# Performance work log

Hardware: AMD Instinct MI355X
Metric: run time of the kernel (lower is better)

Reference implementation:

```python
import jax, jax.numpy as jnp
import numpy as np

B, N, D = 4, 1024, 1024
H, DH = 16, 64            # heads, dim_head; inner_dim = H*DH = D
CTX_N, CTX_D = 77, 768    # CLIP text context
FF_IN, FF_HID = 8 * D, 4 * D  # GEGLU: proj to 2*4*D, gate to 4*D
EPS = 1e-5
SCALE = DH ** -0.5
NL = 256                  # 2**8 levels for all quantizers
ZP_QKV = 128.0            # asymmetric 8-bit zero point for q/k/v
ZP_W = 0.0                # always_zero=True for softmax-weight quantizer


def _round_ste(t):
    return t + jax.lax.stop_gradient(jnp.round(t) - t)


def _fake_quant(x, delta, zp):
    xq = jnp.clip(_round_ste(x / delta) + zp, 0.0, NL - 1.0)
    return (xq - zp) * delta


def _ln(x, w, b):
    m = x.mean(-1, keepdims=True)
    v = x.var(-1, keepdims=True)
    return (x - m) * jax.lax.rsqrt(v + EPS) * w + b


def _split_heads(t):  # [b, n, h*d] -> [b, h, n, d]
    b, n, _ = t.shape
    return t.reshape(b, n, H, DH).transpose(0, 2, 1, 3)


def _attn(x, ctx, wq, wk, wv, wo, bo, dq, dk, dv, dw):
    q = _split_heads(x @ wq)
    k = _split_heads(ctx @ wk)
    v = _split_heads(ctx @ wv)
    qq = _fake_quant(q, dq, ZP_QKV)
    kk = _fake_quant(k, dk, ZP_QKV)
    sim = jnp.einsum('bhid,bhjd->bhij', qq, kk) * SCALE
    attn = jax.nn.softmax(sim, axis=-1)
    aw = _fake_quant(attn, dw, ZP_W)
    vv = _fake_quant(v, dv, ZP_QKV)
    out = jnp.einsum('bhij,bhjd->bhid', aw, vv)
    b, _, n, _ = out.shape
    out = out.transpose(0, 2, 1, 3).reshape(b, n, H * DH)
    return out @ wo + bo


def _geglu_ff(x, w1, b1, w2, b2):
    h = x @ w1 + b1
    a, g = jnp.split(h, 2, axis=-1)
    return (a * jax.nn.gelu(g, approximate=False)) @ w2 + b2


def setup_inputs() -> dict:
    key = jax.random.key(0)
    ks = jax.random.split(key, 16)
    w = lambda i, shp, s: jax.random.normal(ks[i], shp, jnp.float32) * s
    sD = D ** -0.5
    sC = CTX_D ** -0.5
    return {
        'x': jax.random.normal(ks[0], (B, N, D), jnp.float32),
        'context': jax.random.normal(ks[1], (B, CTX_N, CTX_D), jnp.float32),
        'norm1_w': jnp.ones((D,), jnp.float32), 'norm1_b': jnp.zeros((D,), jnp.float32),
        'norm2_w': jnp.ones((D,), jnp.float32), 'norm2_b': jnp.zeros((D,), jnp.float32),
        'norm3_w': jnp.ones((D,), jnp.float32), 'norm3_b': jnp.zeros((D,), jnp.float32),
        'a1_wq': w(2, (D, D), sD), 'a1_wk': w(3, (D, D), sD), 'a1_wv': w(4, (D, D), sD),
        'a1_wo': w(5, (D, D), sD), 'a1_bo': jnp.zeros((D,), jnp.float32),
        'a2_wq': w(6, (D, D), sD), 'a2_wk': w(7, (CTX_D, D), sC), 'a2_wv': w(8, (CTX_D, D), sC),
        'a2_wo': w(9, (D, D), sD), 'a2_bo': jnp.zeros((D,), jnp.float32),
        'ff_w1': w(10, (D, FF_IN), sD), 'ff_b1': jnp.zeros((FF_IN,), jnp.float32),
        'ff_w2': w(11, (FF_HID, D), FF_HID ** -0.5), 'ff_b2': jnp.zeros((D,), jnp.float32),
        'd1_q': jnp.asarray(0.02, jnp.float32), 'd1_k': jnp.asarray(0.02, jnp.float32),
        'd1_v': jnp.asarray(0.02, jnp.float32), 'd1_w': jnp.asarray(1.0 / 255.0, jnp.float32),
        'd2_q': jnp.asarray(0.02, jnp.float32), 'd2_k': jnp.asarray(0.02, jnp.float32),
        'd2_v': jnp.asarray(0.02, jnp.float32), 'd2_w': jnp.asarray(1.0 / 255.0, jnp.float32),
    }


def reference(x, context, norm1_w, norm1_b, norm2_w, norm2_b, norm3_w, norm3_b,
              a1_wq, a1_wk, a1_wv, a1_wo, a1_bo,
              a2_wq, a2_wk, a2_wv, a2_wo, a2_bo,
              ff_w1, ff_b1, ff_w2, ff_b2,
              d1_q, d1_k, d1_v, d1_w, d2_q, d2_k, d2_v, d2_w):
    # attn1: quantized self-attention
    x = _attn(_ln(x, norm1_w, norm1_b), _ln(x, norm1_w, norm1_b),
              a1_wq, a1_wk, a1_wv, a1_wo, a1_bo, d1_q, d1_k, d1_v, d1_w) + x
    # attn2: quantized cross-attention with text context
    x = _attn(_ln(x, norm2_w, norm2_b), context,
              a2_wq, a2_wk, a2_wv, a2_wo, a2_bo, d2_q, d2_k, d2_v, d2_w) + x
    # GEGLU feed-forward
    x = _geglu_ff(_ln(x, norm3_w, norm3_b), ff_w1, ff_b1, ff_w2, ff_b2) + x
    return x
```

## Files before the change

### kernel.cpp

```cpp
#include <hip/hip_runtime.h>
#include <math.h>


typedef unsigned short u16;
typedef __attribute__((ext_vector_type(8))) short short8;
typedef __attribute__((ext_vector_type(4))) float f32x4;

__device__ inline float b2f(u16 v) { return __uint_as_float(((unsigned)v) << 16); }
__device__ inline u16 f2b(float f) {
  unsigned u = __float_as_uint(f);
  unsigned r = u + 0x7fffu + ((u >> 16) & 1u);
  return (u16)(r >> 16);
}

__device__ inline void glds16(const u16* g, u16* l) {
  __builtin_amdgcn_global_load_lds(
      (const __attribute__((address_space(1))) void*)g,
      (__attribute__((address_space(3))) void*)l, 16, 0, 0);
}

__global__ __launch_bounds__(256) void transpose_k(const float* __restrict__ in,
                                                   u16* __restrict__ out,
                                                   int R, int C) {
  __shared__ float t[32][33];
  int tx = threadIdx.x & 31, ty = threadIdx.x >> 5;
  int c0 = blockIdx.x * 32, r0 = blockIdx.y * 32;
#pragma unroll
  for (int i = 0; i < 32; i += 8)
    t[ty + i][tx] = in[(size_t)(r0 + ty + i) * C + c0 + tx];
  __syncthreads();
#pragma unroll
  for (int i = 0; i < 32; i += 8)
    out[(size_t)(c0 + ty + i) * R + r0 + tx] = f2b(t[tx][ty + i]);
}

struct TrBatch { const float* in[4]; u16* out[4]; int R[4]; };
__global__ __launch_bounds__(256) void transpose4_k(TrBatch a) {
  int z = blockIdx.z;
  const float* in = a.in[z];
  u16* out = a.out[z];
  int R = a.R[z];
  int r0 = blockIdx.y * 32;
  if (r0 >= R) return;
  __shared__ float t[32][33];
  int tx = threadIdx.x & 31, ty = threadIdx.x >> 5;
  int c0 = blockIdx.x * 32;
#pragma unroll
  for (int i = 0; i < 32; i += 8)
    t[ty + i][tx] = in[(size_t)(r0 + ty + i) * 1024 + c0 + tx];
  __syncthreads();
#pragma unroll
  for (int i = 0; i < 32; i += 8)
    out[(size_t)(c0 + ty + i) * R + r0 + tx] = f2b(t[tx][ty + i]);
}

__global__ __launch_bounds__(256) void tr16_k(const u16* __restrict__ in,
                                              u16* __restrict__ out, int NK,
                                              int NKP) {
  __shared__ u16 t[32][33];
  int tx = threadIdx.x & 31, ty = threadIdx.x >> 5;
  int n0 = blockIdx.x * 32, c0 = blockIdx.y * 32, b = blockIdx.z;
  const u16* ib = in + (size_t)b * NK * 1024;
  u16* ob = out + (size_t)b * 1024 * NKP;
#pragma unroll
  for (int i = 0; i < 32; i += 8) {
    int n = n0 + ty + i;
    n = n < NK ? n : NK - 1;
    t[ty + i][tx] = ib[(size_t)n * 1024 + c0 + tx];
  }
  __syncthreads();
#pragma unroll
  for (int i = 0; i < 32; i += 8)
    ob[(size_t)(c0 + ty + i) * NKP + n0 + tx] = t[tx][ty + i];
}

__global__ __launch_bounds__(256) void cast_k(const float* __restrict__ in,
                                              u16* __restrict__ out) {
  int i = (blockIdx.x * 256 + threadIdx.x) * 4;
  float4 v = *(const float4*)(in + i);
  out[i + 0] = f2b(v.x);
  out[i + 1] = f2b(v.y);
  out[i + 2] = f2b(v.z);
  out[i + 3] = f2b(v.w);
}

__global__ __launch_bounds__(256) void ln_k(const float* __restrict__ X,
                                            const float* __restrict__ W,
                                            const float* __restrict__ Bi,
                                            u16* __restrict__ Out) {
  const int row = blockIdx.x, tid = threadIdx.x;
  float4 x = *(const float4*)(X + (size_t)row * 1024 + tid * 4);
  float s = x.x + x.y + x.z + x.w;
  float s2 = x.x * x.x + x.y * x.y + x.z * x.z + x.w * x.w;
#pragma unroll
  for (int off = 32; off >= 1; off >>= 1) {
    s += __shfl_down(s, off);
    s2 += __shfl_down(s2, off);
  }
  __shared__ float red[8];
  int wave = tid >> 6, lane = tid & 63;
  if (lane == 0) { red[wave] = s; red[4 + wave] = s2; }
  __syncthreads();
  s = red[0] + red[1] + red[2] + red[3];
  s2 = red[4] + red[5] + red[6] + red[7];
  float mean = s * 0.0009765625f;
  float var = s2 * 0.0009765625f - mean * mean;
  float rs = rsqrtf(var + 1e-5f);
  float4 w = *(const float4*)(W + tid * 4);
  float4 b = *(const float4*)(Bi + tid * 4);
  u16* orow = Out + (size_t)row * 1024 + tid * 4;
  orow[0] = f2b((x.x - mean) * rs * w.x + b.x);
  orow[1] = f2b((x.y - mean) * rs * w.y + b.y);
  orow[2] = f2b((x.z - mean) * rs * w.z + b.z);
  orow[3] = f2b((x.w - mean) * rs * w.w + b.w);
}

template <int EPI, int TM>
__global__ __launch_bounds__(256, 2) void gemm_bt(
    const u16* __restrict__ A, int lda, const u16* __restrict__ Bt, int ldb,
    void* __restrict__ Cp, int ldc, const float* __restrict__ bias,
    const float* __restrict__ res, int ldr, const float* __restrict__ dp,
    const float* __restrict__ dp2, const float* __restrict__ dp3,
    size_t segsz, int M, int N, int K) {
  __shared__ __align__(16) u16 As[TM * 64];
  __shared__ __align__(16) u16 Bs[128 * 64];
  const int tid = threadIdx.x;
  const int lane = tid & 63, wave = tid >> 6;
  const int qd = lane >> 4, cl = lane & 15;
  const int wm = (wave & 1) * (TM / 2), wn = (wave >> 1) << 6;
  const int m0 = blockIdx.x * TM, n0 = blockIdx.y * 128;

  f32x4 acc[TM / 32][4];
  const f32x4 zero = {0.f, 0.f, 0.f, 0.f};
#pragma unroll
  for (int i = 0; i < TM / 32; i++)
#pragma unroll
    for (int j = 0; j < 4; j++) acc[i][j] = zero;

  for (int k0 = 0; k0 < K; k0 += 64) {
    __syncthreads();
#pragma unroll
    for (int it = 0; it < TM / 32; ++it) {
      int ch = it * 256 + tid;
      int r = ch >> 3, cc = (ch & 7) << 3;
      int gr = m0 + r;
      gr = gr < M ? gr : M - 1;
      glds16(A + (size_t)gr * lda + k0 + cc, As + ch * 8);
    }
#pragma unroll
    for (int it = 0; it < 4; ++it) {
      int ch = it * 256 + tid;
      int r = ch >> 3, cc = (ch & 7) << 3;
      glds16(Bt + (size_t)(n0 + r) * ldb + k0 + cc, Bs + ch * 8);
    }
    __syncthreads();
#pragma unroll
    for (int ks = 0; ks < 64; ks += 32) {
      short8 af[TM / 32], bf[4];
#pragma unroll
      for (int t = 0; t < TM / 32; t++)
        af[t] = *(const short8*)(As + (wm + t * 16 + cl) * 64 + ks + qd * 8);
#pragma unroll
      for (int t = 0; t < 4; t++)
        bf[t] = *(const short8*)(Bs + (wn + t * 16 + cl) * 64 + ks + qd * 8);
#pragma unroll
      for (int mt = 0; mt < TM / 32; mt++)
#pragma unroll
        for (int nt = 0; nt < 4; nt++)
          acc[mt][nt] = __builtin_amdgcn_mfma_f32_16x16x32_bf16(
              af[mt], bf[nt], acc[mt][nt], 0, 0, 0);
    }
  }

  float dscale = 1.f;
  u16* qbase = (u16*)Cp;
  if constexpr (EPI == 0) dscale = 1.0f / dp[0];
  if constexpr (EPI == 2) {
    int seg = n0 >> 10;
    const float* ds = (seg == 0) ? dp : ((seg == 1) ? dp2 : dp3);
    dscale = 1.0f / ds[0];
    qbase = (u16*)Cp + (size_t)seg * segsz;
  }
#pragma unroll
  for (int mt = 0; mt < TM / 32; ++mt) {
#pragma unroll
    for (int r = 0; r < 4; ++r) {
      int row = m0 + wm + mt * 16 + qd * 4 + r;
      if (row >= M) continue;
#pragma unroll
      for (int nt = 0; nt < 4; ++nt) {
        int col = n0 + wn + nt * 16 + cl;
        float v = acc[mt][nt][r];
        if constexpr (EPI == 0) {
          float xq = rintf(v * dscale) + 128.f;
          xq = fminf(fmaxf(xq, 0.f), 255.f);
          qbase[(size_t)row * ldc + col] = f2b(xq - 128.f);
        } else if constexpr (EPI == 2) {
          float xq = rintf(v * dscale) + 128.f;
          xq = fminf(fmaxf(xq, 0.f), 255.f);
          qbase[(size_t)row * ldc + (col & 1023)] = f2b(xq - 128.f);
        } else {
          v += bias[col] + res[(size_t)row * ldr + col];
          ((float*)Cp)[(size_t)row * ldc + col] = v;
        }
      }
    }
  }
}

#define VMW(n) asm volatile("s_waitcnt vmcnt(" #n ")" ::: "memory")
#define LGKM0() asm volatile("s_waitcnt lgkmcnt(0)" ::: "memory")
#define SBAR() __builtin_amdgcn_s_barrier()
#define SCHED0() __builtin_amdgcn_sched_barrier(0)

#define ST_A(P, MH, K0)                                                      \
  do {                                                                       \
    _Pragma("unroll") for (int it = 0; it < 2; ++it) {                       \
      int r_ = (MH) * 128 + it * 64 + sr;                                    \
      glds16(Ag + (size_t)(m0 + r_) * 1024 + (K0) + ((sc ^ (r_ & 7)) << 3),  \
             As + (P) * 16384 + r_ * 64 + (sc << 3));                        \
    }                                                                        \
  } while (0)

#define ST_B(P, BH, K0)                                                      \
  do {                                                                       \
    _Pragma("unroll") for (int it = 0; it < 2; ++it) {                       \
      int r_ = it * 64 + sr;                                                 \
      glds16(W1t + (size_t)((BH) * 4096 + n0 + r_) * 1024 + (K0) +           \
                 ((sc ^ (r_ & 7)) << 3),                                     \
             Bs + (P) * 16384 + ((BH) * 128 + r_) * 64 + (sc << 3));         \
    }                                                                        \
  } while (0)

#define RD_A(P, MH)                                                          \
  do {                                                                       \
    _Pragma("unroll") for (int mf = 0; mf < 4; ++mf) {                       \
      int row_ = (MH) * 128 + wr * 64 + mf * 16 + cl;                        \
      _Pragma("unroll") for (int ks = 0; ks < 2; ++ks)                       \
        af[mf * 2 + ks] = *(const short8*)(As + (P) * 16384 + row_ * 64 +    \
                                           (((ks * 4 + qd) ^ (cl & 7)) << 3)); \
    }                                                                        \
  } while (0)

#define RD_B(P, NH)                                                          \
  do {                                                                       \
    _Pragma("unroll") for (int nf = 0; nf < 2; ++nf) {                       \
      int j_ = (NH) * 128 + wc * 32 + nf * 16 + cl;                          \
      _Pragma("unroll") for (int ks = 0; ks < 2; ++ks)                       \
        bf[nf * 2 + ks] = *(const short8*)(Bs + (P) * 16384 + j_ * 64 +      \
                                           (((ks * 4 + qd) ^ (cl & 7)) << 3)); \
    }                                                                        \
  } while (0)

#define MFMA_Q(MH, NH)                                                       \
  do {                                                                       \
    _Pragma("unroll") for (int mf = 0; mf < 4; ++mf)                         \
      _Pragma("unroll") for (int nf = 0; nf < 2; ++nf)                       \
        _Pragma("unroll") for (int ks = 0; ks < 2; ++ks)                     \
          acc[(MH) * 4 + mf][(NH) * 2 + nf] =                                \
              __builtin_amdgcn_mfma_f32_16x16x32_bf16(                       \
                  af[mf * 2 + ks], bf[nf * 2 + ks],                          \
                  acc[(MH) * 4 + mf][(NH) * 2 + nf], 0, 0, 0);               \
  } while (0)

#define KTILE(P, KN, LAST)                                                   \
  do {                                                                       \
                                            \
    RD_A(P, 0);                                                              \
    RD_B(P, 0);                                                              \
    if (!(LAST)) ST_A((P) ^ 1, 0, KN);                                       \
    SBAR();                                                                  \
    LGKM0();                                                                 \
    SCHED0();                                                                \
    __builtin_amdgcn_s_setprio(1);                                           \
    MFMA_Q(0, 0);                                                            \
    __builtin_amdgcn_s_setprio(0);                                           \
    SCHED0();                                                                \
    if (!(LAST)) { VMW(4); } else { VMW(2); }                                \
    SBAR();                                                                  \
                              \
    RD_A(P, 1);                                                              \
    if (!(LAST)) ST_B((P) ^ 1, 0, KN);                                       \
    SBAR();                                                                  \
    LGKM0();                                                                 \
    SCHED0();                                                                \
    __builtin_amdgcn_s_setprio(1);                                           \
    MFMA_Q(1, 0);                                                            \
    __builtin_amdgcn_s_setprio(0);                                           \
    SCHED0();                                                                \
    if (!(LAST)) { VMW(4); } else { VMW(0); }                                \
    SBAR();                                                                  \
                              \
    RD_B(P, 1);                                                              \
    if (!(LAST)) ST_A((P) ^ 1, 1, KN);                                       \
    SBAR();                                                                  \
    LGKM0();                                                                 \
    SCHED0();                                                                \
    __builtin_amdgcn_s_setprio(1);                                           \
    MFMA_Q(1, 1);                                                            \
    __builtin_amdgcn_s_setprio(0);                                           \
    SCHED0();                                                                \
    SBAR();                                                                  \
             \
    RD_A(P, 0);                                                              \
    if (!(LAST)) ST_B((P) ^ 1, 1, KN);                                       \
    SBAR();                                                                  \
    LGKM0();                                                                 \
    SCHED0();                                                                \
    __builtin_amdgcn_s_setprio(1);                                           \
    MFMA_Q(0, 1);                                                            \
    __builtin_amdgcn_s_setprio(0);                                           \
    SCHED0();                                                                \
    if (!(LAST)) { VMW(4); }                                                 \
    SBAR();                                                                  \
  } while (0)

__global__ __launch_bounds__(512, 1) void ff1_geglu8_k(
    const u16* __restrict__ Ag, const u16* __restrict__ W1t,
    const float* __restrict__ b1, u16* __restrict__ gg) {
  __shared__ __align__(16) u16 smem[65536];
  u16* As = smem;
  u16* Bs = smem + 32768;
  const int tid = threadIdx.x;
  const int lane = tid & 63, wave = tid >> 6;
  const int qd = lane >> 4, cl = lane & 15;
  const int wr = wave >> 2, wc = wave & 3;
  const int m0 = blockIdx.x * 256;
  const int n0 = blockIdx.y * 128;
  const int sr = tid >> 3, sc = tid & 7;

  f32x4 acc[8][4];
  const f32x4 zero = {0.f, 0.f, 0.f, 0.f};
#pragma unroll
  for (int i = 0; i < 8; ++i)
#pragma unroll
    for (int j = 0; j < 4; ++j) acc[i][j] = zero;
  short8 af[8], bf[4];

  ST_A(0, 0, 0);
  ST_B(0, 0, 0);
  ST_A(0, 1, 0);
  ST_B(0, 1, 0);
  VMW(4);
  SBAR();
  SCHED0();

  int p = 0;
#pragma unroll 1
  for (int t = 0; t < 15; ++t) {
    KTILE(p, (t + 1) * 64, 0);
    p ^= 1;
  }
  KTILE(1, 0, 1);

#pragma unroll
  for (int i = 0; i < 8; ++i) {
    const int row = m0 + (i >> 2) * 128 + wr * 64 + (i & 3) * 16 + qd * 4;
#pragma unroll
    for (int nf = 0; nf < 2; ++nf) {
      const int col = n0 + wc * 32 + nf * 16 + cl;
      const float ba = b1[col];
      const float bg = b1[4096 + col];
#pragma unroll
      for (int r = 0; r < 4; ++r) {
        float a = acc[i][nf][r] + ba;
        float g = acc[i][2 + nf][r] + bg;
        float ge = 0.5f * g * (1.0f + erff(g * 0.70710678118654752f));
        gg[(size_t)(row + r) * 4096 + col] = f2b(a * ge);
      }
    }
  }
}

__global__ __launch_bounds__(256, 4) void attn_k(
    const u16* __restrict__ Q, const u16* __restrict__ Kb,
    const u16* __restrict__ VbT, u16* __restrict__ O,
    const float* dqp, const float* dkp, const float* dvp, const float* dwp,
    int NK, int NKP) {
  __shared__ __align__(16) u16 Ks[64 * 64];
  __shared__ __align__(16) u16 VTs[64 * 64];
  __shared__ __align__(16) u16 Ps[4][16 * 72];
  const int tid = threadIdx.x;
  const int lane = tid & 63, wave = tid >> 6;
  const int qd = lane >> 4, cl = lane & 15;
  const int b = blockIdx.z, h = blockIdx.y, qt = blockIdx.x;
  const float sscale = dqp[0] * dkp[0] * 0.125f;
  const float oscale = dwp[0] * dvp[0];
  const float inv_dw = 1.0f / dwp[0];
  const f32x4 zero = {0.f, 0.f, 0.f, 0.f};

  short8 qf[2][2];
#pragma unroll
  for (int g = 0; g < 2; ++g) {
    const u16* qrow =
        Q + (size_t)(b * 1024 + qt * 128 + g * 64 + wave * 16 + cl) * 1024 +
        h * 64;
    qf[g][0] = *(const short8*)(qrow + qd * 8);
    qf[g][1] = *(const short8*)(qrow + 32 + qd * 8);
  }

  const u16* kbase = Kb + (size_t)(b * NK) * 1024 + h * 64;
  const u16* vtbase = VbT + ((size_t)b * 1024 + h * 64) * NKP;
  const int r_st = tid >> 3, c_st = (tid & 7) << 3;

  float m_s[2] = {-1e30f, -1e30f}, l_s[2] = {0.f, 0.f};
  for (int j0 = 0; j0 < NK; j0 += 64) {
    __syncthreads();
#pragma unroll
    for (int it = 0; it < 2; ++it) {
      int r = it * 32 + r_st;
      int j = j0 + r;
      j = j < NK ? j : NK - 1;
      glds16(kbase + (size_t)j * 1024 + c_st, Ks + (it * 256 + tid) * 8);
    }
    __syncthreads();
    const bool full = (j0 + 64 <= NK);
#pragma unroll
    for (int g = 0; g < 2; ++g) {
      float sc[16];
#pragma unroll
      for (int nt = 0; nt < 4; ++nt) {
        short8 kf0 = *(const short8*)(Ks + (nt * 16 + cl) * 64 + qd * 8);
        short8 kf1 = *(const short8*)(Ks + (nt * 16 + cl) * 64 + 32 + qd * 8);
        f32x4 st = zero;
        st = __builtin_amdgcn_mfma_f32_16x16x32_bf16(kf0, qf[g][0], st, 0, 0, 0);
        st = __builtin_amdgcn_mfma_f32_16x16x32_bf16(kf1, qf[g][1], st, 0, 0, 0);
#pragma unroll
        for (int r = 0; r < 4; ++r) {
          int key = j0 + nt * 16 + qd * 4 + r;
          sc[nt * 4 + r] = (full || key < NK) ? st[r] * sscale : -1e30f;
        }
      }
      float mx = sc[0];
#pragma unroll
      for (int i = 1; i < 16; ++i) mx = fmaxf(mx, sc[i]);
      mx = fmaxf(mx, __shfl_xor(mx, 16));
      mx = fmaxf(mx, __shfl_xor(mx, 32));
      float mn = fmaxf(m_s[g], mx);
      float ss = 0.f;
#pragma unroll
      for (int i = 0; i < 16; ++i) ss += __expf(sc[i] - mn);
      ss += __shfl_xor(ss, 16);
      ss += __shfl_xor(ss, 32);
      l_s[g] = l_s[g] * __expf(m_s[g] - mn) + ss;
      m_s[g] = mn;
    }
  }
  float il_s[2] = {1.0f / l_s[0], 1.0f / l_s[1]};

  f32x4 oacc[2][4];
#pragma unroll
  for (int g = 0; g < 2; ++g)
#pragma unroll
    for (int t = 0; t < 4; t++) oacc[g][t] = zero;

  for (int j0 = 0; j0 < NK; j0 += 64) {
    __syncthreads();
#pragma unroll
    for (int it = 0; it < 2; ++it) {
      int r = it * 32 + r_st;
      int j = j0 + r;
      j = j < NK ? j : NK - 1;
      glds16(kbase + (size_t)j * 1024 + c_st, Ks + (it * 256 + tid) * 8);
      glds16(vtbase + (size_t)r * NKP + j0 + c_st, VTs + (it * 256 + tid) * 8);
    }
    __syncthreads();
    const bool full = (j0 + 64 <= NK);
#pragma unroll
    for (int g = 0; g < 2; ++g) {
#pragma unroll
      for (int nt = 0; nt < 4; ++nt) {
        short8 kf0 = *(const short8*)(Ks + (nt * 16 + cl) * 64 + qd * 8);
        short8 kf1 = *(const short8*)(Ks + (nt * 16 + cl) * 64 + 32 + qd * 8);
        f32x4 st = zero;
        st = __builtin_amdgcn_mfma_f32_16x16x32_bf16(kf0, qf[g][0], st, 0, 0, 0);
        st = __builtin_amdgcn_mfma_f32_16x16x32_bf16(kf1, qf[g][1], st, 0, 0, 0);
        u16 pk[4];
#pragma unroll
        for (int r = 0; r < 4; ++r) {
          int key = j0 + nt * 16 + qd * 4 + r;
          float aw = 0.f;
          if (full || key < NK) {
            float attn = __expf(st[r] * sscale - m_s[g]) * il_s[g];
            aw = fminf(fmaxf(rintf(attn * inv_dw), 0.f), 255.f);
          }
          pk[r] = f2b(aw);
        }
        uint2 pv;
        pv.x = (unsigned)pk[0] | ((unsigned)pk[1] << 16);
        pv.y = (unsigned)pk[2] | ((unsigned)pk[3] << 16);
        *(uint2*)(&Ps[wave][cl * 72 + nt * 16 + qd * 4]) = pv;
      }
#pragma unroll
      for (int ks = 0; ks < 2; ++ks) {
        short8 pf = *(const short8*)(&Ps[wave][cl * 72 + ks * 32 + qd * 8]);
#pragma unroll
        for (int dt = 0; dt < 4; ++dt) {
          short8 vf =
              *(const short8*)(VTs + (dt * 16 + cl) * 64 + ks * 32 + qd * 8);
          oacc[g][dt] = __builtin_amdgcn_mfma_f32_16x16x32_bf16(
              pf, vf, oacc[g][dt], 0, 0, 0);
        }
      }
    }
  }
#pragma unroll
  for (int g = 0; g < 2; ++g)
#pragma unroll
    for (int dt = 0; dt < 4; ++dt)
#pragma unroll
      for (int r = 0; r < 4; r++) {
        size_t addr = (size_t)(b * 1024 + qt * 128 + g * 64 + wave * 16 +
                               qd * 4 + r) * 1024 +
                      h * 64 + dt * 16 + cl;
        O[addr] = f2b(oacc[g][dt][r] * oscale);
      }
}

extern "C" void kernel_launch(void* const* d_in, const int* in_sizes, int n_in,
                              void* d_out, int out_size, void* d_ws,
                              size_t ws_size, hipStream_t stream) {
  (void)in_sizes; (void)n_in; (void)out_size; (void)ws_size;
  const float* x    = (const float*)d_in[0];
  const float* ctx  = (const float*)d_in[1];
  const float* n1w  = (const float*)d_in[2];
  const float* n1b  = (const float*)d_in[3];
  const float* n2w  = (const float*)d_in[4];
  const float* n2b  = (const float*)d_in[5];
  const float* n3w  = (const float*)d_in[6];
  const float* n3b  = (const float*)d_in[7];
  const float* a1wq = (const float*)d_in[8];
  const float* a1wk = (const float*)d_in[9];
  const float* a1wv = (const float*)d_in[10];
  const float* a1wo = (const float*)d_in[11];
  const float* a1bo = (const float*)d_in[12];
  const float* a2wq = (const float*)d_in[13];
  const float* a2wk = (const float*)d_in[14];
  const float* a2wv = (const float*)d_in[15];
  const float* a2wo = (const float*)d_in[16];
  const float* a2bo = (const float*)d_in[17];
  const float* ffw1 = (const float*)d_in[18];
  const float* ffb1 = (const float*)d_in[19];
  const float* ffw2 = (const float*)d_in[20];
  const float* ffb2 = (const float*)d_in[21];
  const float* d1q = (const float*)d_in[22];
  const float* d1k = (const float*)d_in[23];
  const float* d1v = (const float*)d_in[24];
  const float* d1w = (const float*)d_in[25];
  const float* d2q = (const float*)d_in[26];
  const float* d2k = (const float*)d_in[27];
  const float* d2v = (const float*)d_in[28];
  const float* d2w = (const float*)d_in[29];

  char* ws = (char*)d_ws;
  const size_t MB = 1u << 20;
  u16* W    = (u16*)(ws + 0 * MB);
  u16* lnb  = (u16*)(ws + 16 * MB);
  u16* qb   = (u16*)(ws + 24 * MB);
  u16* kb   = (u16*)(ws + 32 * MB);
  u16* vb   = (u16*)(ws + 40 * MB);
  u16* vbT  = (u16*)(ws + 48 * MB);
  u16* ao   = (u16*)(ws + 56 * MB);
  float* x1 = (float*)(ws + 64 * MB);
  u16* k2b  = (u16*)(ws + 32 * MB);
  u16* v2b  = k2b + 308 * 1024;
  u16* vbTc = (u16*)(ws + 34 * MB);
  u16* ctxb = (u16*)(ws + 35 * MB);
  u16* gg   = (u16*)(ws + 24 * MB);

  u16* WT0 = W;
  u16* WT1 = (u16*)(ws + 2 * MB);
  u16* WT2 = (u16*)(ws + 4 * MB);
  u16* WT3 = (u16*)(ws + 6 * MB);
  u16* WT3c = WT2 + 1024 * 768;

  dim3 T256(256);
  {
    TrBatch tb;
    tb.in[0] = a1wq; tb.out[0] = WT0; tb.R[0] = 1024;
    tb.in[1] = a1wk; tb.out[1] = WT1; tb.R[1] = 1024;
    tb.in[2] = a1wv; tb.out[2] = WT2; tb.R[2] = 1024;
    tb.in[3] = a1wo; tb.out[3] = WT3; tb.R[3] = 1024;
    transpose4_k<<<dim3(32, 32, 4), T256, 0, stream>>>(tb);
  }
  ln_k<<<4096, T256, 0, stream>>>(x, n1w, n1b, lnb);
  gemm_bt<2, 128><<<dim3(32, 24), T256, 0, stream>>>(
      lnb, 1024, WT0, 1024, qb, 1024, nullptr, nullptr, 0, d1q, d1k, d1v,
      (size_t)4096 * 1024, 4096, 3072, 1024);
  tr16_k<<<dim3(32, 32, 4), T256, 0, stream>>>(vb, vbT, 1024, 1024);
  attn_k<<<dim3(8, 16, 4), T256, 0, stream>>>(qb, kb, vbT, ao, d1q, d1k, d1v,
                                              d1w, 1024, 1024);
  gemm_bt<1, 64><<<dim3(64, 8), T256, 0, stream>>>(
      ao, 1024, WT3, 1024, x1, 1024, a1bo, x, 1024, nullptr, nullptr, nullptr,
      0, 4096, 1024, 1024);
  {
    TrBatch tb;
    tb.in[0] = a2wq; tb.out[0] = WT0; tb.R[0] = 1024;
    tb.in[1] = a2wo; tb.out[1] = WT1; tb.R[1] = 1024;
    tb.in[2] = a2wk; tb.out[2] = WT2;  tb.R[2] = 768;
    tb.in[3] = a2wv; tb.out[3] = WT3c; tb.R[3] = 768;
    transpose4_k<<<dim3(32, 32, 4), T256, 0, stream>>>(tb);
  }
  ln_k<<<4096, T256, 0, stream>>>(x1, n2w, n2b, lnb);
  cast_k<<<231, T256, 0, stream>>>(ctx, ctxb);
  gemm_bt<0, 64><<<dim3(64, 8), T256, 0, stream>>>(
      lnb, 1024, WT0, 1024, qb, 1024, nullptr, nullptr, 0, d2q, nullptr,
      nullptr, 0, 4096, 1024, 1024);
  gemm_bt<2, 64><<<dim3(5, 16), T256, 0, stream>>>(
      ctxb, 768, WT2, 768, k2b, 1024, nullptr, nullptr, 0, d2k, d2v, nullptr,
      (size_t)308 * 1024, 308, 2048, 768);
  tr16_k<<<dim3(3, 32, 4), T256, 0, stream>>>(v2b, vbTc, 77, 128);
  attn_k<<<dim3(8, 16, 4), T256, 0, stream>>>(qb, k2b, vbTc, ao, d2q, d2k, d2v,
                                              d2w, 77, 128);
  gemm_bt<1, 64><<<dim3(64, 8), T256, 0, stream>>>(
      ao, 1024, WT1, 1024, x1, 1024, a2bo, x1, 1024, nullptr, nullptr, nullptr,
      0, 4096, 1024, 1024);
  transpose_k<<<dim3(256, 32), T256, 0, stream>>>(ffw1, W, 1024, 8192);
  ln_k<<<4096, T256, 0, stream>>>(x1, n3w, n3b, lnb);
  ff1_geglu8_k<<<dim3(16, 32), dim3(512), 0, stream>>>(lnb, W, ffb1, gg);
  transpose_k<<<dim3(32, 128), T256, 0, stream>>>(ffw2, W, 4096, 1024);
  gemm_bt<1, 64><<<dim3(64, 8), T256, 0, stream>>>(
      gg, 4096, W, 4096, d_out, 1024, ffb2, x1, 1024, nullptr, nullptr,
      nullptr, 0, 4096, 1024, 4096);
}
```

Before: 578.5 us.

## Restructure quantized attention: 64-row tiles, XOR-swizzled LDS, exp2 with folded normalization

The attention kernel now handles 64 query rows per block instead of 128, and the grid doubles to keep total work constant. This raises block count and parallelism, but each K/V tile is loaded by twice as many blocks. K and V^T tiles are stored in LDS with an XOR swizzle on the 16-byte column chunks to reduce bank conflicts on fragment reads. The softmax uses exp2 with the log2e factor folded into the score scale, and the 1/l normalization and 1/dw quantization scale are folded into a single subtracted bias, so the second pass needs one FMA plus exp2. The clamp at zero and the bf16 rounding of integer weights are dropped, since exp is non-negative and integers up to 255 are exact in bf16.

Result: faster. 546.1 us (-5.6%).

```diff
diff --git a/kernel.cpp b/kernel.cpp
--- a/kernel.cpp
+++ b/kernel.cpp
@@ -11,6 +11,14 @@
   unsigned u = __float_as_uint(f);
   unsigned r = u + 0x7fffu + ((u >> 16) & 1u);
   return (u16)(r >> 16);
+}
+
+__device__ inline float exp2_fast(float x) {
+#if __has_builtin(__builtin_amdgcn_exp2f)
+  return __builtin_amdgcn_exp2f(x);
+#else
+  return __expf(x * 0.6931471805599453f);
+#endif
 }
 
 __device__ inline void glds16(const u16* g, u16* l) {
@@ -384,26 +392,73 @@
   const int lane = tid & 63, wave = tid >> 6;
   const int qd = lane >> 4, cl = lane & 15;
   const int b = blockIdx.z, h = blockIdx.y, qt = blockIdx.x;
-  const float sscale = dqp[0] * dkp[0] * 0.125f;
+  const float ss2 = dqp[0] * dkp[0] * 0.125f * 1.4426950408889634f;
   const float oscale = dwp[0] * dvp[0];
   const float inv_dw = 1.0f / dwp[0];
   const f32x4 zero = {0.f, 0.f, 0.f, 0.f};
 
-  short8 qf[2][2];
-#pragma unroll
-  for (int g = 0; g < 2; ++g) {
+  short8 qf0, qf1;
+  {
     const u16* qrow =
-        Q + (size_t)(b * 1024 + qt * 128 + g * 64 + wave * 16 + cl) * 1024 +
-        h * 64;
-    qf[g][0] = *(const short8*)(qrow + qd * 8);
-    qf[g][1] = *(const short8*)(qrow + 32 + qd * 8);
+        Q + (size_t)(b * 1024 + qt * 64 + wave * 16 + cl) * 1024 + h * 64;
+    qf0 = *(const short8*)(qrow + qd * 8);
+    qf1 = *(const short8*)(qrow + 32 + qd * 8);
   }
 
   const u16* kbase = Kb + (size_t)(b * NK) * 1024 + h * 64;
   const u16* vtbase = VbT + ((size_t)b * 1024 + h * 64) * NKP;
-  const int r_st = tid >> 3, c_st = (tid & 7) << 3;
-
-  float m_s[2] = {-1e30f, -1e30f}, l_s[2] = {0.f, 0.f};
+  const int r_st = tid >> 3;
+  const int c_sw = (((tid & 7) ^ (r_st & 7)) << 3);
+
+  float m_s = -1e30f, l_s = 0.f;
+  for (int j0 = 0; j0 < NK; j0 += 64) {
+    __syncthreads();
+#pragma unroll
+    for (int it = 0; it < 2; ++it) {
+      int j = j0 + it * 32 + r_st;
+      j = j < NK ? j : NK - 1;
+      glds16(kbase + (size_t)j * 1024 + c_sw, Ks + (it * 256 + tid) * 8);
+    }
+    __syncthreads();
+    const bool full = (j0 + 64 <= NK);
+    float sc[16];
+#pragma unroll
+    for (int nt = 0; nt < 4; ++nt) {
+      const int row = nt * 16 + cl, sw = cl & 7;
+      short8 kf0 = *(const short8*)(Ks + row * 64 + ((qd ^ sw) << 3));
+      short8 kf1 = *(const short8*)(Ks + row * 64 + (((4 | qd) ^ sw) << 3));
+      f32x4 st = zero;
+      st = __builtin_amdgcn_mfma_f32_16x16x32_bf16(kf0, qf0, st, 0, 0, 0);
+      st = __builtin_amdgcn_mfma_f32_16x16x32_bf16(kf1, qf1, st, 0, 0, 0);
+#pragma unroll
+      for (int r = 0; r < 4; ++r) {
+        int key = j0 + nt * 16 + qd * 4 + r;
+        sc[nt * 4 + r] = (full || key < NK) ? st[r] * ss2 : -1e30f;
+      }
+    }
+    float t0 = fmaxf(fmaxf(sc[0], sc[1]), sc[2]);
+    float t1 = fmaxf(fmaxf(sc[3], sc[4]), sc[5]);
+    float t2 = fmaxf(fmaxf(sc[6], sc[7]), sc[8]);
+    float t3 = fmaxf(fmaxf(sc[9], sc[10]), sc[11]);
+    float t4 = fmaxf(fmaxf(sc[12], sc[13]), sc[14]);
+    float mx = fmaxf(fmaxf(fmaxf(t0, t1), fmaxf(t2, t3)), fmaxf(t4, sc[15]));
+    mx = fmaxf(mx, __shfl_xor(mx, 16));
+    mx = fmaxf(mx, __shfl_xor(mx, 32));
+    float mn = fmaxf(m_s, mx);
+    float ss = 0.f;
+#pragma unroll
+    for (int i = 0; i < 16; ++i) ss += exp2_fast(sc[i] - mn);
+    ss += __shfl_xor(ss, 16);
+    ss += __shfl_xor(ss, 32);
+    l_s = l_s * exp2_fast(m_s - mn) + ss;
+    m_s = mn;
+  }
+  const float mb = m_s + log2f(l_s) - log2f(inv_dw);
+
+  f32x4 oacc[4];
+#pragma unroll
+  for (int t = 0; t < 4; t++) oacc[t] = zero;
+
   for (int j0 = 0; j0 < NK; j0 += 64) {
     __syncthreads();
 #pragma unroll
@@ -411,110 +466,57 @@
       int r = it * 32 + r_st;
       int j = j0 + r;
       j = j < NK ? j : NK - 1;
-      glds16(kbase + (size_t)j * 1024 + c_st, Ks + (it * 256 + tid) * 8);
+      glds16(kbase + (size_t)j * 1024 + c_sw, Ks + (it * 256 + tid) * 8);
+      glds16(vtbase + (size_t)r * NKP + j0 + c_sw, VTs + (it * 256 + tid) * 8);
     }
     __syncthreads();
     const bool full = (j0 + 64 <= NK);
 #pragma unroll
-    for (int g = 0; g < 2; ++g) {
-      float sc[16];
-#pragma unroll
-      for (int nt = 0; nt < 4; ++nt) {
-        short8 kf0 = *(const short8*)(Ks + (nt * 16 + cl) * 64 + qd * 8);
-        short8 kf1 = *(const short8*)(Ks + (nt * 16 + cl) * 64 + 32 + qd * 8);
-        f32x4 st = zero;
-        st = __builtin_amdgcn_mfma_f32_16x16x32_bf16(kf0, qf[g][0], st, 0, 0, 0);
-        st = __builtin_amdgcn_mfma_f32_16x16x32_bf16(kf1, qf[g][1], st, 0, 0, 0);
-#pragma unroll
-        for (int r = 0; r < 4; ++r) {
-          int key = j0 + nt * 16 + qd * 4 + r;
-          sc[nt * 4 + r] = (full || key < NK) ? st[r] * sscale : -1e30f;
+    for (int nt = 0; nt < 4; ++nt) {
+      const int row = nt * 16 + cl, sw = cl & 7;
+      short8 kf0 = *(const short8*)(Ks + row * 64 + ((qd ^ sw) << 3));
+      short8 kf1 = *(const short8*)(Ks + row * 64 + (((4 | qd) ^ sw) << 3));
+      f32x4 st = zero;
+      st = __builtin_amdgcn_mfma_f32_16x16x32_bf16(kf0, qf0, st, 0, 0, 0);
+      st = __builtin_amdgcn_mfma_f32_16x16x32_bf16(kf1, qf1, st, 0, 0, 0);
+      unsigned a[4];
+#pragma unroll
+      for (int r = 0; r < 4; ++r) {
+        int key = j0 + nt * 16 + qd * 4 + r;
+        float aw = 0.f;
+        if (full || key < NK) {
+          float e = exp2_fast(__builtin_fmaf(st[r], ss2, -mb));
+          aw = fminf(rintf(e), 255.f);
         }
+        a[r] = __float_as_uint(aw);
       }
-      float mx = sc[0];
-#pragma unroll
-      for (int i = 1; i < 16; ++i) mx = fmaxf(mx, sc[i]);
-      mx = fmaxf(mx, __shfl_xor(mx, 16));
-      mx = fmaxf(mx, __shfl_xor(mx, 32));
-      float mn = fmaxf(m_s[g], mx);
-      float ss = 0.f;
-#pragma unroll
-      for (int i = 0; i < 16; ++i) ss += __expf(sc[i] - mn);
-      ss += __shfl_xor(ss, 16);
-      ss += __shfl_xor(ss, 32);
-      l_s[g] = l_s[g] * __expf(m_s[g] - mn) + ss;
-      m_s[g] = mn;
-    }
-  }
-  float il_s[2] = {1.0f / l_s[0], 1.0f / l_s[1]};
-
-  f32x4 oacc[2][4];
-#pragma unroll
-  for (int g = 0; g < 2; ++g)
-#pragma unroll
-    for (int t = 0; t < 4; t++) oacc[g][t] = zero;
-
-  for (int j0 = 0; j0 < NK; j0 += 64) {
-    __syncthreads();
-#pragma unroll
-    for (int it = 0; it < 2; ++it) {
-      int r = it * 32 + r_st;
-      int j = j0 + r;
-      j = j < NK ? j : NK - 1;
-      glds16(kbase + (size_t)j * 1024 + c_st, Ks + (it * 256 + tid) * 8);
-      glds16(vtbase + (size_t)r * NKP + j0 + c_st, VTs + (it * 256 + tid) * 8);
-    }
-    __syncthreads();
-    const bool full = (j0 + 64 <= NK);
-#pragma unroll
-    for (int g = 0; g < 2; ++g) {
-#pragma unroll
-      for (int nt = 0; nt < 4; ++nt) {
-        short8 kf0 = *(const short8*)(Ks + (nt * 16 + cl) * 64 + qd * 8);
-        short8 kf1 = *(const short8*)(Ks + (nt * 16 + cl) * 64 + 32 + qd * 8);
-        f32x4 st = zero;
-        st = __builtin_amdgcn_mfma_f32_16x16x32_bf16(kf0, qf[g][0], st, 0, 0, 0);
-        st = __builtin_amdgcn_mfma_f32_16x16x32_bf16(kf1, qf[g][1], st, 0, 0, 0);
-        u16 pk[4];
-#pragma unroll
-        for (int r = 0; r < 4; ++r) {
-          int key = j0 + nt * 16 + qd * 4 + r;
-          float aw = 0.f;
-          if (full || key < NK) {
-            float attn = __expf(st[r] * sscale - m_s[g]) * il_s[g];
-            aw = fminf(fmaxf(rintf(attn * inv_dw), 0.f), 255.f);
-          }
-          pk[r] = f2b(aw);
-        }
-        uint2 pv;
-        pv.x = (unsigned)pk[0] | ((unsigned)pk[1] << 16);
-        pv.y = (unsigned)pk[2] | ((unsigned)pk[3] << 16);
-        *(uint2*)(&Ps[wave][cl * 72 + nt * 16 + qd * 4]) = pv;
+      uint2 pv;
+      pv.x = (a[0] >> 16) | (a[1] & 0xffff0000u);
+      pv.y = (a[2] >> 16) | (a[3] & 0xffff0000u);
+      *(uint2*)(&Ps[wave][cl * 72 + nt * 16 + qd * 4]) = pv;
+    }
+#pragma unroll
+    for (int ks = 0; ks < 2; ++ks) {
+      short8 pf = *(const short8*)(&Ps[wave][cl * 72 + ks * 32 + qd * 8]);
+#pragma unroll
+      for (int dt = 0; dt < 4; ++dt) {
+        const int vrow = dt * 16 + cl;
+        short8 vf = *(const short8*)(VTs + vrow * 64 +
+                                     (((ks * 4 + qd) ^ (cl & 7)) << 3));
+        oacc[dt] = __builtin_amdgcn_mfma_f32_16x16x32_bf16(pf, vf, oacc[dt],
+                                                           0, 0, 0);
       }
-#pragma unroll
-      for (int ks = 0; ks < 2; ++ks) {
-        short8 pf = *(const short8*)(&Ps[wave][cl * 72 + ks * 32 + qd * 8]);
-#pragma unroll
-        for (int dt = 0; dt < 4; ++dt) {
-          short8 vf =
-              *(const short8*)(VTs + (dt * 16 + cl) * 64 + ks * 32 + qd * 8);
-          oacc[g][dt] = __builtin_amdgcn_mfma_f32_16x16x32_bf16(
-              pf, vf, oacc[g][dt], 0, 0, 0);
-        }
-      }
-    }
-  }
-#pragma unroll
-  for (int g = 0; g < 2; ++g)
-#pragma unroll
-    for (int dt = 0; dt < 4; ++dt)
-#pragma unroll
-      for (int r = 0; r < 4; r++) {
-        size_t addr = (size_t)(b * 1024 + qt * 128 + g * 64 + wave * 16 +
-                               qd * 4 + r) * 1024 +
-                      h * 64 + dt * 16 + cl;
-        O[addr] = f2b(oacc[g][dt][r] * oscale);
-      }
+    }
+  }
+#pragma unroll
+  for (int dt = 0; dt < 4; ++dt)
+#pragma unroll
+    for (int r = 0; r < 4; r++) {
+      size_t addr =
+          (size_t)(b * 1024 + qt * 64 + wave * 16 + qd * 4 + r) * 1024 +
+          h * 64 + dt * 16 + cl;
+      O[addr] = f2b(oacc[dt][r] * oscale);
+    }
 }
 
 extern "C" void kernel_launch(void* const* d_in, const int* in_sizes, int n_in,
@@ -588,8 +590,8 @@
       lnb, 1024, WT0, 1024, qb, 1024, nullptr, nullptr, 0, d1q, d1k, d1v,
       (size_t)4096 * 1024, 4096, 3072, 1024);
   tr16_k<<<dim3(32, 32, 4), T256, 0, stream>>>(vb, vbT, 1024, 1024);
-  attn_k<<<dim3(8, 16, 4), T256, 0, stream>>>(qb, kb, vbT, ao, d1q, d1k, d1v,
-                                              d1w, 1024, 1024);
+  attn_k<<<dim3(16, 16, 4), T256, 0, stream>>>(qb, kb, vbT, ao, d1q, d1k, d1v,
+                                               d1w, 1024, 1024);
   gemm_bt<1, 64><<<dim3(64, 8), T256, 0, stream>>>(
       ao, 1024, WT3, 1024, x1, 1024, a1bo, x, 1024, nullptr, nullptr, nullptr,
       0, 4096, 1024, 1024);
@@ -610,8 +612,8 @@
       ctxb, 768, WT2, 768, k2b, 1024, nullptr, nullptr, 0, d2k, d2v, nullptr,
       (size_t)308 * 1024, 308, 2048, 768);
   tr16_k<<<dim3(3, 32, 4), T256, 0, stream>>>(v2b, vbTc, 77, 128);
-  attn_k<<<dim3(8, 16, 4), T256, 0, stream>>>(qb, k2b, vbTc, ao, d2q, d2k, d2v,
-                                              d2w, 77, 128);
+  attn_k<<<dim3(16, 16, 4), T256, 0, stream>>>(qb, k2b, vbTc, ao, d2q, d2k,
+                                               d2v, d2w, 77, 128);
   gemm_bt<1, 64><<<dim3(64, 8), T256, 0, stream>>>(
       ao, 1024, WT1, 1024, x1, 1024, a2bo, x1, 1024, nullptr, nullptr, nullptr,
       0, 4096, 1024, 1024);
```
